# Kernel tuning notes

Hardware: AMD Instinct MI355X
Metric: run time of the kernel (lower is better)

## Reference

```python
import jax, jax.numpy as jnp
from jax import lax
import numpy as np

NSAMPLE = 32  # from __init__


def setup_inputs() -> dict:
    key = jax.random.key(0)
    k1, k2 = jax.random.split(key)
    B, N, C = 8, 16384, 128
    xyz = jax.random.uniform(k1, (B, N, 3), dtype=jnp.float32)
    points = jax.random.normal(k2, (B, N, C), dtype=jnp.float32)
    return {"npoint": 1024, "radius": 0.2, "xyz": xyz, "points": points}


def furthest_point_sample(xyz, npoint):
    # xyz: (B, N, 3) -> (B, npoint) int32 indices; CUDA impl seeds at index 0
    B, N, _ = xyz.shape
    d0 = jnp.full((B, N), 1e10, dtype=xyz.dtype)
    far0 = jnp.zeros((B,), dtype=jnp.int32)
    barange = jnp.arange(B)

    def step(carry, _):
        d, far = carry
        centroid = xyz[barange, far]                      # (B, 3)
        dist = jnp.sum((xyz - centroid[:, None, :]) ** 2, axis=-1)  # (B, N)
        d = jnp.minimum(d, dist)
        far_new = jnp.argmax(d, axis=-1).astype(jnp.int32)
        return (d, far_new), far

    _, idxs = lax.scan(step, (d0, far0), None, length=npoint)
    return idxs.T  # (B, npoint)


def ball_query(radius, nsample, xyz, new_xyz):
    # returns idx (B, S, nsample): first <=nsample point indices within radius,
    # remaining slots filled with the first found index (0 if none found)
    B, N, _ = xyz.shape
    S = new_xyz.shape[1]
    # squared distances via GEMM to avoid (B,S,N,3) temp
    d2 = (jnp.sum(new_xyz ** 2, -1)[:, :, None]
          + jnp.sum(xyz ** 2, -1)[:, None, :]
          - 2.0 * jnp.einsum('bsd,bnd->bsn', new_xyz, xyz))  # (B, S, N)
    mask = d2 < radius * radius
    arangeN = jnp.arange(N, dtype=jnp.int32)
    key = jnp.where(mask, arangeN, N)                 # invalid -> sentinel N
    neg_vals, pos = lax.top_k(-key, nsample)          # smallest keys first
    valid = (-neg_vals) < N                           # (B, S, nsample)
    first = pos[..., 0:1]
    fill = jnp.where(valid[..., 0:1], first, 0)
    idx = jnp.where(valid, pos, fill).astype(jnp.int32)
    return idx


def _group(feat, idx):
    # feat: (B, N, C), idx: (B, S, K) -> (B, S, K, C)
    return jax.vmap(lambda f, i: f[i])(feat, idx)


def reference(npoint, radius, xyz, points):
    fps_idx = furthest_point_sample(xyz, npoint)              # (B, npoint)
    new_xyz = jax.vmap(lambda x, i: x[i])(xyz, fps_idx)       # (B, npoint, 3)
    idx = ball_query(radius, NSAMPLE, xyz, new_xyz)           # (B, npoint, K)
    grouped_xyz = _group(xyz, idx) - new_xyz[:, :, None, :]   # (B, npoint, K, 3)
    new_points = _group(points, idx)                          # use_xyz=False
    return new_xyz, new_points, idx, grouped_xyz
```

## Files before the change

### kernel.cpp

```cpp
#include <hip/hip_runtime.h>

#define B 8
#define N 16384
#define NPOINT 1024
#define NSAMPLE 32
#define CDIM 128
#define CELLS 4096

#define OFF_NEWXYZ 0
#define OFF_NEWPTS (B * NPOINT * 3)
#define OFF_IDX    (OFF_NEWPTS + B * NPOINT * NSAMPLE * CDIM)
#define OFF_GXYZ   (OFF_IDX + B * NPOINT * NSAMPLE)

typedef unsigned long long u64;

template <int CTRL>
__device__ __forceinline__ u64 mindpp_u64(u64 k) {
    const int lo = (int)(unsigned)(k & 0xffffffffull);
    const int hi = (int)(unsigned)(k >> 32);
    const int lo2 = __builtin_amdgcn_update_dpp(lo, lo, CTRL, 0xf, 0xf, false);
    const int hi2 = __builtin_amdgcn_update_dpp(hi, hi, CTRL, 0xf, 0xf, false);
    const u64 kt = ((u64)(unsigned)hi2 << 32) | (unsigned)lo2;
    return kt < k ? kt : k;
}

__device__ __forceinline__ int spread3(int v) {
    return (v & 1) | ((v & 2) << 2) | ((v & 4) << 4) | ((v & 8) << 6);
}

__global__ __launch_bounds__(1024) void sort_kernel(const float* __restrict__ xyz,
                                                    float* __restrict__ sorted) {
    const int b = blockIdx.x;
    const int t = threadIdx.x;
    const float* xb = xyz + (size_t)b * N * 3;

    __shared__ unsigned int hist[CELLS];
    __shared__ unsigned int waveS[16];

#pragma unroll
    for (int i = 0; i < CELLS / 1024; ++i) hist[i * 1024 + t] = 0;
    __syncthreads();

    int cell[16];
#pragma unroll
    for (int k = 0; k < 16; ++k) {
        const int n = k * 1024 + t;
        const float x = xb[n * 3 + 0];
        const float y = xb[n * 3 + 1];
        const float z = xb[n * 3 + 2];
        int cx = (int)(x * 16.0f); cx = cx < 0 ? 0 : (cx > 15 ? 15 : cx);
        int cy = (int)(y * 16.0f); cy = cy < 0 ? 0 : (cy > 15 ? 15 : cy);
        int cz = (int)(z * 16.0f); cz = cz < 0 ? 0 : (cz > 15 ? 15 : cz);
        cell[k] = spread3(cx) | (spread3(cy) << 1) | (spread3(cz) << 2);
        atomicAdd(&hist[cell[k]], 1u);
    }
    __syncthreads();

    const unsigned h0 = hist[4 * t + 0], h1 = hist[4 * t + 1],
                   h2 = hist[4 * t + 2], h3 = hist[4 * t + 3];
    const unsigned sum4 = h0 + h1 + h2 + h3;
    const int wid = t >> 6, lane = t & 63;
    unsigned inc = sum4;
#pragma unroll
    for (int off = 1; off < 64; off <<= 1) {
        const unsigned v = __shfl_up(inc, off);
        if (lane >= off) inc += v;
    }
    if (lane == 63) waveS[wid] = inc;
    __syncthreads();
    unsigned wbase = 0;
    {
        unsigned ws = (lane < 16) ? waveS[lane] : 0u;
        unsigned wi = ws;
#pragma unroll
        for (int off = 1; off < 16; off <<= 1) {
            const unsigned v = __shfl_up(wi, off);
            if (lane >= off) wi += v;
        }
        wbase = __shfl(wi - ws, wid);
    }
    const unsigned base = wbase + (inc - sum4);
    __syncthreads();
    hist[4 * t + 0] = base;
    hist[4 * t + 1] = base + h0;
    hist[4 * t + 2] = base + h0 + h1;
    hist[4 * t + 3] = base + h0 + h1 + h2;
    __syncthreads();

    float4* sb = (float4*)sorted + (size_t)b * N;
#pragma unroll
    for (int k = 0; k < 16; ++k) {
        const int n = k * 1024 + t;
        const float x = xb[n * 3 + 0];
        const float y = xb[n * 3 + 1];
        const float z = xb[n * 3 + 2];
        const unsigned pos = atomicAdd(&hist[cell[k]], 1u);
        sb[pos] = make_float4(x, y, z, (float)n);
    }
}

__global__ __launch_bounds__(1024) void fps_kernel(const float* __restrict__ xyz,
                                                   const float* __restrict__ sorted,
                                                   float* out) {
#pragma clang fp contract(off)
    const int b = blockIdx.x;
    const int t = threadIdx.x;
    const float* xb = xyz + (size_t)b * N * 3;
    const float4* sb = (const float4*)sorted + (size_t)b * N;

    __shared__ u64 swkey[2][16];
    const int wid = t >> 6;
    const int lane = t & 63;

    float d[16];
    float lox = 1e30f, hix = -1e30f, loy = 1e30f, hiy = -1e30f, loz = 1e30f, hiz = -1e30f;
#pragma unroll
    for (int k = 0; k < 16; ++k) {
        const float4 v = sb[t * 16 + k];
        lox = fminf(lox, v.x); hix = fmaxf(hix, v.x);
        loy = fminf(loy, v.y); hiy = fmaxf(hiy, v.y);
        loz = fminf(loz, v.z); hiz = fmaxf(hiz, v.z);
        d[k] = 1e10f;
    }
    float mval = 1e10f;
    int   mn   = 0;
    __syncthreads();

    float* nxo = out + OFF_NEWXYZ + (size_t)b * NPOINT * 3;
    int far = 0;

    for (int s = 0; s < NPOINT; ++s) {
        const int fs = __builtin_amdgcn_readfirstlane(far);
        const float cx = xb[fs * 3 + 0];
        const float cy = xb[fs * 3 + 1];
        const float cz = xb[fs * 3 + 2];
        if (t == 0) {
            nxo[s * 3 + 0] = cx;
            nxo[s * 3 + 1] = cy;
            nxo[s * 3 + 2] = cz;
        }
        if (s == NPOINT - 1) break;

        const float ax = fmaxf(fmaxf(__fsub_rn(lox, cx), __fsub_rn(cx, hix)), 0.0f);
        const float ay = fmaxf(fmaxf(__fsub_rn(loy, cy), __fsub_rn(cy, hiy)), 0.0f);
        const float az = fmaxf(fmaxf(__fsub_rn(loz, cz), __fsub_rn(cz, hiz)), 0.0f);
        const float md2 = __fadd_rn(__fadd_rn(__fmul_rn(ax, ax), __fmul_rn(ay, ay)),
                                    __fmul_rn(az, az));
        const bool ex = !(md2 > __fmul_rn(mval, 1.0001f));
        if (__ballot(ex) != 0ull) {
            if (ex) {
                float bv = -1.0f;
                int bn2 = 0x7fffffff;
#pragma unroll
                for (int k = 0; k < 16; ++k) {
                    const float4 v = sb[t * 16 + k];
                    const float dx = __fsub_rn(v.x, cx);
                    const float dy = __fsub_rn(v.y, cy);
                    const float dz = __fsub_rn(v.z, cz);
                    const float dist = __fadd_rn(
                        __fadd_rn(__fmul_rn(dx, dx), __fmul_rn(dy, dy)),
                        __fmul_rn(dz, dz));
                    const float dk = fminf(d[k], dist);
                    d[k] = dk;
                    const int nk = (int)v.w;
                    if (dk > bv) { bv = dk; bn2 = nk; }
                    else if (dk == bv && nk < bn2) { bn2 = nk; }
                }
                mval = bv;
                mn = bn2;
            }
        }
        u64 key = ((u64)(unsigned)(~__float_as_uint(mval)) << 14) | (unsigned)mn;
        key = mindpp_u64<0x111>(key);
        key = mindpp_u64<0x112>(key);
        key = mindpp_u64<0x114>(key);
        key = mindpp_u64<0x118>(key);
        key = mindpp_u64<0x142>(key);
        key = mindpp_u64<0x143>(key);
        if (lane == 63) swkey[s & 1][wid] = key;
        __syncthreads();
        u64 kk = swkey[s & 1][lane & 15];
        kk = mindpp_u64<0x111>(kk);
        kk = mindpp_u64<0x112>(kk);
        kk = mindpp_u64<0x114>(kk);
        kk = mindpp_u64<0x118>(kk);
        const int lo15 = __builtin_amdgcn_readlane((int)(unsigned)(kk & 0xffffffffull), 15);
        far = lo15 & 16383;
    }
}

__global__ __launch_bounds__(256) void ballq_kernel(const float* __restrict__ xyz,
                                                    const float* __restrict__ radius_p,
                                                    float* out) {
    const int wib = threadIdx.x >> 6;
    const int lane = threadIdx.x & 63;
    const int gw = blockIdx.x * 4 + wib;
    const int b = gw >> 10;
    const int s = gw & 1023;

    const float r = radius_p[0];
    const float r2 = __fmul_rn(r, r);

    const float* xb = xyz + (size_t)b * N * 3;
    const float* nx = out + OFF_NEWXYZ + (size_t)(b * NPOINT + s) * 3;
    const float c0 = nx[0], c1 = nx[1], c2 = nx[2];
    const float ss_s = __fadd_rn(__fadd_rn(__fmul_rn(c0, c0), __fmul_rn(c1, c1)),
                                 __fmul_rn(c2, c2));

    float* oidx = out + OFF_IDX + (size_t)(b * NPOINT + s) * NSAMPLE;
    float* ogx  = out + OFF_GXYZ + (size_t)(b * NPOINT + s) * NSAMPLE * 3;

    int filled = 0;
    int first = -1;
    for (int n0 = 0; n0 < N; n0 += 64) {
        const int n = n0 + lane;
        const float x = xb[n * 3 + 0];
        const float y = xb[n * 3 + 1];
        const float z = xb[n * 3 + 2];
        const float ssx = __fadd_rn(__fadd_rn(__fmul_rn(x, x), __fmul_rn(y, y)),
                                    __fmul_rn(z, z));
        const float dot = __fadd_rn(__fadd_rn(__fmul_rn(c0, x), __fmul_rn(c1, y)),
                                    __fmul_rn(c2, z));
        const float d2 = __fsub_rn(__fadd_rn(ss_s, ssx), __fmul_rn(2.0f, dot));
        const bool in = d2 < r2;
        const unsigned long long m = __ballot(in);
        if (first < 0 && m != 0ull) first = n0 + (int)__builtin_ctzll(m);
        if (in) {
            const int pos = filled + (int)__popcll(m & ((1ull << lane) - 1ull));
            if (pos < NSAMPLE) {
                oidx[pos] = (float)n;
                ogx[pos * 3 + 0] = __fsub_rn(x, c0);
                ogx[pos * 3 + 1] = __fsub_rn(y, c1);
                ogx[pos * 3 + 2] = __fsub_rn(z, c2);
            }
        }
        filled += (int)__popcll(m);
        if (filled >= NSAMPLE) break;
    }
    if (filled < NSAMPLE) {
        if (first < 0) first = 0;
        const float fx = xb[first * 3 + 0];
        const float fy = xb[first * 3 + 1];
        const float fz = xb[first * 3 + 2];
        const float g0 = __fsub_rn(fx, c0);
        const float g1 = __fsub_rn(fy, c1);
        const float g2 = __fsub_rn(fz, c2);
        for (int pos = filled + lane; pos < NSAMPLE; pos += 64) {
            oidx[pos] = (float)first;
            ogx[pos * 3 + 0] = g0;
            ogx[pos * 3 + 1] = g1;
            ogx[pos * 3 + 2] = g2;
        }
    }
}

__global__ __launch_bounds__(256) void gather_kernel(const float* __restrict__ points,
                                                     float* out) {
    const int blk = blockIdx.x;
    const int w = threadIdx.x >> 6;
    const int lane = threadIdx.x & 63;
    const int b = blk >> 10;

    const float* oidx = out + OFF_IDX + (size_t)blk * NSAMPLE;
    const float* pb = points + (size_t)b * N * CDIM;
    float* onp = out + OFF_NEWPTS + (size_t)blk * NSAMPLE * CDIM;

#pragma unroll
    for (int i = 0; i < 8; ++i) {
        const int slot = w * 8 + i;
        const int n = (int)oidx[slot];
        const float2 v = *(const float2*)(pb + (size_t)n * CDIM + lane * 2);
        *(float2*)(onp + (size_t)slot * CDIM + lane * 2) = v;
    }
}

extern "C" void kernel_launch(void* const* d_in, const int* in_sizes, int n_in,
                              void* d_out, int out_size, void* d_ws, size_t ws_size,
                              hipStream_t stream) {
    const float* xyz = (const float*)d_in[2];
    const float* points = (const float*)d_in[3];
    const float* radius = (const float*)d_in[1];
    float* out = (float*)d_out;

    float* sorted = out + OFF_NEWPTS;

    hipLaunchKernelGGL(sort_kernel, dim3(B), dim3(1024), 0, stream, xyz, sorted);
    hipLaunchKernelGGL(fps_kernel, dim3(B), dim3(1024), 0, stream, xyz, sorted, out);
    hipLaunchKernelGGL(ballq_kernel, dim3((B * NPOINT) / 4), dim3(256), 0, stream, xyz, radius, out);
    hipLaunchKernelGGL(gather_kernel, dim3(B * NPOINT), dim3(256), 0, stream, points, out);
}
```

Measured before the change: 1.549 ms.

## Redistribute FPS distance updates across all threads via shared work queue

Instead of each thread updating its own 16 sorted points only when its bounding box may be affected (leaving most threads idle), active segments are pushed into a shared queue. The per-point update work is then spread across all 1024 threads, with distances stored as packed keys in LDS and per-segment maxima gathered by atomicMin. This targets load imbalance in the FPS loop, at the cost of an extra barrier, LDS atomics and 128KB of shared memory per block.

```diff
diff --git a/kernel.cpp b/kernel.cpp
--- a/kernel.cpp
+++ b/kernel.cpp
@@ -108,22 +108,28 @@
     const float* xb = xyz + (size_t)b * N * 3;
     const float4* sb = (const float4*)sorted + (size_t)b * N;
 
+    __shared__ u64 pkey[N];
+    __shared__ u64 segkey[1024];
+    __shared__ unsigned short queue[1024];
+    __shared__ unsigned qc[2];
     __shared__ u64 swkey[2][16];
+
     const int wid = t >> 6;
     const int lane = t & 63;
 
-    float d[16];
     float lox = 1e30f, hix = -1e30f, loy = 1e30f, hiy = -1e30f, loz = 1e30f, hiz = -1e30f;
+    const u64 dinit = (u64)(unsigned)(~__float_as_uint(1e10f)) << 14;
 #pragma unroll
     for (int k = 0; k < 16; ++k) {
         const float4 v = sb[t * 16 + k];
         lox = fminf(lox, v.x); hix = fmaxf(hix, v.x);
         loy = fminf(loy, v.y); hiy = fmaxf(hiy, v.y);
         loz = fminf(loz, v.z); hiz = fmaxf(hiz, v.z);
-        d[k] = 1e10f;
-    }
+        pkey[t * 16 + k] = dinit | (unsigned)(int)v.w;
+    }
+    if (t < 2) qc[t] = 0;
+    u64 rkey = ~0ull;
     float mval = 1e10f;
-    int   mn   = 0;
     __syncthreads();
 
     float* nxo = out + OFF_NEWXYZ + (size_t)b * NPOINT * 3;
@@ -147,30 +153,39 @@
         const float md2 = __fadd_rn(__fadd_rn(__fmul_rn(ax, ax), __fmul_rn(ay, ay)),
                                     __fmul_rn(az, az));
         const bool ex = !(md2 > __fmul_rn(mval, 1.0001f));
-        if (__ballot(ex) != 0ull) {
-            if (ex) {
-                float bv = -1.0f;
-                int bn2 = 0x7fffffff;
-#pragma unroll
-                for (int k = 0; k < 16; ++k) {
-                    const float4 v = sb[t * 16 + k];
-                    const float dx = __fsub_rn(v.x, cx);
-                    const float dy = __fsub_rn(v.y, cy);
-                    const float dz = __fsub_rn(v.z, cz);
-                    const float dist = __fadd_rn(
-                        __fadd_rn(__fmul_rn(dx, dx), __fmul_rn(dy, dy)),
-                        __fmul_rn(dz, dz));
-                    const float dk = fminf(d[k], dist);
-                    d[k] = dk;
-                    const int nk = (int)v.w;
-                    if (dk > bv) { bv = dk; bn2 = nk; }
-                    else if (dk == bv && nk < bn2) { bn2 = nk; }
-                }
-                mval = bv;
-                mn = bn2;
-            }
-        }
-        u64 key = ((u64)(unsigned)(~__float_as_uint(mval)) << 14) | (unsigned)mn;
+        if (t == 0) qc[(s + 1) & 1] = 0;
+        if (ex) {
+            segkey[t] = ~0ull;
+            const unsigned pos = atomicAdd(&qc[s & 1], 1u);
+            queue[pos] = (unsigned short)t;
+        }
+        __syncthreads();
+
+        const unsigned Ltasks = qc[s & 1] << 4;
+        for (unsigned i = t; i < Ltasks; i += 1024) {
+            const int seg = queue[i >> 4];
+            const int p = (seg << 4) | (int)(i & 15u);
+            const u64 ok = pkey[p];
+            const float4 v = sb[p];
+            const float dx = __fsub_rn(v.x, cx);
+            const float dy = __fsub_rn(v.y, cy);
+            const float dz = __fsub_rn(v.z, cz);
+            const float dist = __fadd_rn(
+                __fadd_rn(__fmul_rn(dx, dx), __fmul_rn(dy, dy)),
+                __fmul_rn(dz, dz));
+            const u64 nk = ((u64)(unsigned)(~__float_as_uint(dist)) << 14) |
+                           (ok & 16383ull);
+            const u64 uk = nk > ok ? nk : ok;
+            pkey[p] = uk;
+            atomicMin(&segkey[seg], uk);
+        }
+        __syncthreads();
+
+        if (ex) {
+            rkey = segkey[t];
+            mval = __uint_as_float(~(unsigned)(rkey >> 14));
+        }
+        u64 key = rkey;
         key = mindpp_u64<0x111>(key);
         key = mindpp_u64<0x112>(key);
         key = mindpp_u64<0x114>(key);
```

After: 1.711 ms. 10.4% more time.
